# Performance work log

Measured on AMD Instinct MI355X. Metric: run time of the kernel, lower is better.

## Reference

```python
import jax, jax.numpy as jnp
import numpy as np

N_NODES = 110
C = 4096  # in_channels = hidden = out_channels


def setup_inputs() -> dict:
    key = jax.random.key(0)
    ks = jax.random.split(key, 8)
    x = jax.random.normal(ks[0], (N_NODES, C), dtype=jnp.float32)
    adj = jax.random.randint(ks[1], (N_NODES, N_NODES), 0, 2, dtype=jnp.int32)
    # torch.nn.Linear weights stored [out_features, in_features]
    W2 = jax.random.normal(ks[2], (C, C), dtype=jnp.float32) / np.sqrt(C)
    b2 = jax.random.normal(ks[3], (C,), dtype=jnp.float32) * 0.01
    W1 = jax.random.normal(ks[4], (2 * C, C), dtype=jnp.float32) / np.sqrt(2 * C)
    b1 = jax.random.normal(ks[5], (C,), dtype=jnp.float32) * 0.01
    Wl = jax.random.normal(ks[6], (N_NODES, N_NODES), dtype=jnp.float32) / np.sqrt(N_NODES)
    bl = jax.random.normal(ks[7], (N_NODES,), dtype=jnp.float32) * 0.01
    # note: W1 is stored [in=2C, out=C]; W2 [in=C, out=C]; Wl [in=110, out=110]
    return {"x": x, "adj": adj, "W2": W2, "b2": b2, "W1": W1, "b1": b1, "Wl": Wl, "bl": bl}


def reference(x, adj, W2, b2, W1, b1, Wl, bl):
    # FeatGraphConv: h = lin2(x)
    h = x @ W2 + b2  # [N, C]
    # edge_index.nonzero(): adjacency -> edge list (i=src, j=dst); mean-aggregate
    # h[src] at dst. Dense equivalent: column-normalized mask matmul.
    mask = (adj != 0).astype(x.dtype)  # [N, N]
    deg = mask.sum(axis=0)  # in-degree of each target node j
    aggr = (mask.T @ h) / jnp.maximum(deg, 1.0)[:, None]  # [N, C]; 0 for isolated nodes (PyG mean)
    # update: lin1(cat(h, aggr)) then relu (in RegGNN.forward)
    out = jax.nn.relu(jnp.concatenate([h, aggr], axis=1) @ W1 + b1)  # [N, C]
    # x.t(); lin(110,110); x.t()
    out = (out.T @ Wl.T + bl).T  # [N, C]
    return out
```

## Files before the change

kernel.cpp:

```cpp
#include <hip/hip_runtime.h>
#include <hip/hip_fp16.h>

#define C 4096
#define NN 110
#define MPAD 112
#define BN 128
#define BK 64
#define KCHUNK 512
#define LDSTR 72

typedef _Float16 f16x8 __attribute__((ext_vector_type(8)));
typedef float fx4 __attribute__((ext_vector_type(4)));

__global__ void prep1_kernel(const float* __restrict__ x, _Float16* __restrict__ A1) {
    int idx = blockIdx.x * 256 + threadIdx.x;
    int n = idx >> 12;
    float v = (n < NN) ? x[idx] : 0.f;
    A1[idx] = (_Float16)v;
}

__global__ __launch_bounds__(256, 2)
void mm_kernel(const _Float16* __restrict__ A, const float* __restrict__ B,
               float* __restrict__ Cacc, int lda) {
    __shared__ _Float16 As[MPAD * LDSTR];
    __shared__ _Float16 Bs[BN * LDSTR];

    const int t  = threadIdx.x;
    const int j0 = blockIdx.x * BN;
    const int k0 = blockIdx.y * KCHUNK;
    const int w   = t >> 6;
    const int L   = t & 63;
    const int l15 = L & 15;
    const int q   = L >> 4;

    const int bc  = t & 127;
    const int bgq = t >> 7;

    fx4 acc[7][2];
    #pragma unroll
    for (int mt = 0; mt < 7; ++mt)
        #pragma unroll
        for (int nt = 0; nt < 2; ++nt)
            acc[mt][nt] = (fx4){0.f, 0.f, 0.f, 0.f};

    for (int kc = 0; kc < KCHUNK; kc += BK) {
        {
            int idx = t;
            #pragma unroll
            for (int i = 0; i < 4; ++i) {
                if (idx < MPAD * (BK / 8)) {
                    int row = idx >> 3;
                    int ko  = (idx & 7) << 3;
                    *(f16x8*)(As + row * LDSTR + ko) =
                        *(const f16x8*)(A + (size_t)row * lda + k0 + kc + ko);
                }
                idx += 256;
            }
        }
        {
            #pragma unroll
            for (int p = 0; p < 16; ++p) {
                int r = (bgq * 16 + p) * 2;
                float v0 = B[(size_t)(k0 + kc + r) * C + j0 + bc];
                float v1 = B[(size_t)(k0 + kc + r + 1) * C + j0 + bc];
                union { _Float16 h[2]; unsigned u; } pk;
                pk.h[0] = (_Float16)v0;
                pk.h[1] = (_Float16)v1;
                *(unsigned*)(Bs + bc * LDSTR + r) = pk.u;
            }
        }
        __syncthreads();
        #pragma unroll
        for (int s = 0; s < 2; ++s) {
            const int ko = s * 32 + q * 8;
            f16x8 bfrag[2];
            #pragma unroll
            for (int nt = 0; nt < 2; ++nt)
                bfrag[nt] = *(const f16x8*)(Bs + (w * 32 + nt * 16 + l15) * LDSTR + ko);
            #pragma unroll
            for (int mt = 0; mt < 7; ++mt) {
                f16x8 afrag = *(const f16x8*)(As + (mt * 16 + l15) * LDSTR + ko);
                #pragma unroll
                for (int nt = 0; nt < 2; ++nt)
                    acc[mt][nt] = __builtin_amdgcn_mfma_f32_16x16x32_f16(
                        afrag, bfrag[nt], acc[mt][nt], 0, 0, 0);
            }
        }
        __syncthreads();
    }

    #pragma unroll
    for (int mt = 0; mt < 7; ++mt) {
        #pragma unroll
        for (int nt = 0; nt < 2; ++nt) {
            const int col = j0 + w * 32 + nt * 16 + l15;
            #pragma unroll
            for (int r = 0; r < 4; ++r) {
                int row = mt * 16 + q * 4 + r;
                if (row < NN)
                    atomicAdd(&Cacc[(size_t)row * C + col], acc[mt][nt][r]);
            }
        }
    }
}

__global__ __launch_bounds__(256)
void agg_kernel(const float* __restrict__ h_raw, const int* __restrict__ adj,
                const float* __restrict__ b2, _Float16* __restrict__ A3) {
    __shared__ float hb[NN * 16];
    __shared__ unsigned long long mlo[NN], mhi[NN];
    __shared__ float degs[NN];
    const int t  = threadIdx.x;
    const int c0 = blockIdx.x * 16;

    for (int idx = t; idx < NN * 16; idx += 256) {
        int n = idx >> 4, c = idx & 15;
        float v = h_raw[(size_t)n * C + c0 + c] + b2[c0 + c];
        hb[idx] = v;
        A3[(size_t)n * (2 * C) + c0 + c] = (_Float16)v;
    }
    if (t < 64) {
        int n  = NN + (t >> 5);
        int hs = (t >> 4) & 1;
        int c  = t & 15;
        A3[(size_t)n * (2 * C) + hs * C + c0 + c] = (_Float16)0.f;
    }
    if (t < NN) {
        int j = t;
        unsigned long long lo = 0, hi = 0;
        int dg = 0;
        for (int i = 0; i < 64; ++i) {
            int m = (adj[i * NN + j] != 0);
            lo |= ((unsigned long long)m) << i; dg += m;
        }
        for (int i = 64; i < NN; ++i) {
            int m = (adj[i * NN + j] != 0);
            hi |= ((unsigned long long)m) << (i - 64); dg += m;
        }
        mlo[j] = lo; mhi[j] = hi;
        degs[j] = (float)(dg > 0 ? dg : 1);
    }
    __syncthreads();
    for (int idx = t; idx < NN * 16; idx += 256) {
        int j = idx >> 4, c = idx & 15;
        unsigned long long lo = mlo[j], hi = mhi[j];
        float a = 0.f;
        for (int i = 0; i < 64; ++i)
            if ((lo >> i) & 1) a += hb[i * 16 + c];
        for (int i = 64; i < NN; ++i)
            if ((hi >> (i - 64)) & 1) a += hb[i * 16 + c];
        A3[(size_t)j * (2 * C) + C + c0 + c] = (_Float16)(a / degs[j]);
    }
}

__global__ __launch_bounds__(256)
void fin_kernel(const float* __restrict__ z_raw, const float* __restrict__ b1,
                const float* __restrict__ Wl, const float* __restrict__ bl,
                float* __restrict__ out) {
    __shared__ float zs[NN * 64];
    const int t  = threadIdx.x;
    const int c0 = blockIdx.x * 64;
    const int j  = blockIdx.y * 4 + (t >> 6);
    const int c  = t & 63;

    for (int idx = t; idx < NN * 64; idx += 256) {
        int k = idx >> 6, cc = idx & 63;
        float v = z_raw[(size_t)k * C + c0 + cc] + b1[c0 + cc];
        zs[idx] = fmaxf(v, 0.f);
    }
    __syncthreads();
    if (j < NN) {
        float a = bl[j];
        #pragma unroll 2
        for (int k = 0; k < NN; ++k)
            a += Wl[j * NN + k] * zs[k * 64 + c];
        out[(size_t)j * C + c0 + c] = a;
    }
}

extern "C" void kernel_launch(void* const* d_in, const int* in_sizes, int n_in,
                              void* d_out, int out_size, void* d_ws, size_t ws_size,
                              hipStream_t stream) {
    const float* x   = (const float*)d_in[0];
    const int*   adj = (const int*)d_in[1];
    const float* W2  = (const float*)d_in[2];
    const float* b2  = (const float*)d_in[3];
    const float* W1  = (const float*)d_in[4];
    const float* b1  = (const float*)d_in[5];
    const float* Wl  = (const float*)d_in[6];
    const float* bl  = (const float*)d_in[7];
    float* out = (float*)d_out;

    char* ws = (char*)d_ws;
    float*    h_raw = (float*)(ws);
    float*    z_raw = (float*)(ws + 1802240);
    _Float16* A1    = (_Float16*)(ws + 3604480);
    _Float16* A3    = (_Float16*)(ws + 4521984);

    hipMemsetAsync(d_ws, 0, 3604480, stream);
    prep1_kernel<<<(MPAD * C) / 256, 256, 0, stream>>>(x, A1);
    mm_kernel<<<dim3(C / BN, C / KCHUNK), 256, 0, stream>>>(A1, W2, h_raw, C);
    agg_kernel<<<C / 16, 256, 0, stream>>>(h_raw, adj, b2, A3);
    mm_kernel<<<dim3(C / BN, (2 * C) / KCHUNK), 256, 0, stream>>>(A3, W1, z_raw, 2 * C);
    fin_kernel<<<dim3(C / 64, 28), 256, 0, stream>>>(z_raw, b1, Wl, bl, out);
}
```

Before: 381.5 us.

## Double-buffer GEMM LDS with register prefetch and XOR-swizzled B tile

The GEMM kernel now prefetches the next K-slice of A and B into registers while MFMAs run on the current LDS buffer, then commits into a second LDS buffer. This hides global load latency behind compute. The B tile drops its padded stride in favour of an XOR swizzle to avoid LDS bank conflicts. Smaller changes vectorise the prep and aggregation kernels to two elements per thread and cut fin_kernel's grid so each block reuses its staged z tile for 28 output rows instead of 4. The cost is more registers (32 floats plus A vectors) and double the LDS in the GEMM, which may reduce occupancy.

After: 358.7 us. -6.0%, faster.

```diff
diff --git a/kernel.cpp b/kernel.cpp
--- a/kernel.cpp
+++ b/kernel.cpp
@@ -7,101 +7,139 @@
 #define BN 128
 #define BK 64
 #define KCHUNK 512
+#define NIT (KCHUNK / BK)
 #define LDSTR 72
+#define BSTR 64
 
 typedef _Float16 f16x8 __attribute__((ext_vector_type(8)));
 typedef float fx4 __attribute__((ext_vector_type(4)));
 
-__global__ void prep1_kernel(const float* __restrict__ x, _Float16* __restrict__ A1) {
+__global__ __launch_bounds__(256)
+void prep1_kernel(const float* __restrict__ x, _Float16* __restrict__ A1) {
     int idx = blockIdx.x * 256 + threadIdx.x;
-    int n = idx >> 12;
-    float v = (n < NN) ? x[idx] : 0.f;
-    A1[idx] = (_Float16)v;
+    int n = idx >> 11;
+    union { _Float16 h[2]; unsigned u; } pk;
+    pk.u = 0;
+    if (n < NN) {
+        float2 v = *(const float2*)(x + 2 * (size_t)idx);
+        pk.h[0] = (_Float16)v.x;
+        pk.h[1] = (_Float16)v.y;
+    }
+    ((unsigned*)A1)[idx] = pk.u;
 }
 
 __global__ __launch_bounds__(256, 2)
 void mm_kernel(const _Float16* __restrict__ A, const float* __restrict__ B,
                float* __restrict__ Cacc, int lda) {
-    __shared__ _Float16 As[MPAD * LDSTR];
-    __shared__ _Float16 Bs[BN * LDSTR];
-
-    const int t  = threadIdx.x;
-    const int j0 = blockIdx.x * BN;
-    const int k0 = blockIdx.y * KCHUNK;
-    const int w   = t >> 6;
-    const int L   = t & 63;
-    const int l15 = L & 15;
-    const int q   = L >> 4;
-
-    const int bc  = t & 127;
-    const int bgq = t >> 7;
+    __shared__ _Float16 As[2][MPAD * LDSTR];
+    __shared__ _Float16 Bs[2][BN * BSTR];
+
+    const int t    = threadIdx.x;
+    const int j0   = blockIdx.x * BN;
+    const int k0   = blockIdx.y * KCHUNK;
+    const int w    = t >> 6;
+    const int L    = t & 63;
+    const int l15  = L & 15;
+    const int q    = L >> 4;
+    const int bc   = t & 127;
+    const int bgq  = t >> 7;
+    const int bswz = bc & 7;
+
+    int arow[4], ako[4];
+    bool aval[4];
+#pragma unroll
+    for (int i = 0; i < 4; ++i) {
+        int idx = t + i * 256;
+        aval[i] = (idx < MPAD * (BK / 8));
+        int id2 = aval[i] ? idx : 0;
+        arow[i] = id2 >> 3;
+        ako[i]  = (id2 & 7) << 3;
+    }
 
     fx4 acc[7][2];
-    #pragma unroll
+#pragma unroll
     for (int mt = 0; mt < 7; ++mt)
-        #pragma unroll
+#pragma unroll
         for (int nt = 0; nt < 2; ++nt)
             acc[mt][nt] = (fx4){0.f, 0.f, 0.f, 0.f};
 
-    for (int kc = 0; kc < KCHUNK; kc += BK) {
-        {
-            int idx = t;
-            #pragma unroll
-            for (int i = 0; i < 4; ++i) {
-                if (idx < MPAD * (BK / 8)) {
-                    int row = idx >> 3;
-                    int ko  = (idx & 7) << 3;
-                    *(f16x8*)(As + row * LDSTR + ko) =
-                        *(const f16x8*)(A + (size_t)row * lda + k0 + kc + ko);
-                }
-                idx += 256;
-            }
-        }
-        {
-            #pragma unroll
-            for (int p = 0; p < 16; ++p) {
-                int r = (bgq * 16 + p) * 2;
-                float v0 = B[(size_t)(k0 + kc + r) * C + j0 + bc];
-                float v1 = B[(size_t)(k0 + kc + r + 1) * C + j0 + bc];
-                union { _Float16 h[2]; unsigned u; } pk;
-                pk.h[0] = (_Float16)v0;
-                pk.h[1] = (_Float16)v1;
-                *(unsigned*)(Bs + bc * LDSTR + r) = pk.u;
-            }
-        }
-        __syncthreads();
-        #pragma unroll
+    f16x8 av[4];
+    float bv[32];
+
+#define STAGE(kc_)                                                             \
+    {                                                                          \
+        _Pragma("unroll")                                                      \
+        for (int i = 0; i < 4; ++i)                                            \
+            av[i] = *(const f16x8*)(A + (size_t)arow[i] * lda + (k0 + (kc_)) + ako[i]); \
+        _Pragma("unroll")                                                      \
+        for (int p = 0; p < 16; ++p) {                                         \
+            int r = (bgq * 16 + p) * 2;                                        \
+            bv[2 * p]     = B[(size_t)(k0 + (kc_) + r) * C + j0 + bc];         \
+            bv[2 * p + 1] = B[(size_t)(k0 + (kc_) + r + 1) * C + j0 + bc];     \
+        }                                                                      \
+    }
+
+#define COMMIT(b_)                                                             \
+    {                                                                          \
+        _Pragma("unroll")                                                      \
+        for (int i = 0; i < 4; ++i)                                            \
+            if (aval[i])                                                       \
+                *(f16x8*)(As[b_] + arow[i] * LDSTR + ako[i]) = av[i];          \
+        _Pragma("unroll")                                                      \
+        for (int p = 0; p < 16; ++p) {                                         \
+            int P = bgq * 16 + p;                                              \
+            union { _Float16 h[2]; unsigned u; } pk;                           \
+            pk.h[0] = (_Float16)bv[2 * p];                                     \
+            pk.h[1] = (_Float16)bv[2 * p + 1];                                 \
+            *(unsigned*)(Bs[b_] + bc * BSTR + (((P >> 2) ^ bswz) << 3)         \
+                         + ((P & 3) << 1)) = pk.u;                             \
+        }                                                                      \
+    }
+
+    STAGE(0);
+    COMMIT(0);
+    __syncthreads();
+
+    for (int it = 0; it < NIT; ++it) {
+        if (it + 1 < NIT) STAGE((it + 1) * BK);
+        const int b = it & 1;
+#pragma unroll
         for (int s = 0; s < 2; ++s) {
             const int ko = s * 32 + q * 8;
             f16x8 bfrag[2];
-            #pragma unroll
-            for (int nt = 0; nt < 2; ++nt)
-                bfrag[nt] = *(const f16x8*)(Bs + (w * 32 + nt * 16 + l15) * LDSTR + ko);
-            #pragma unroll
+#pragma unroll
+            for (int nt = 0; nt < 2; ++nt) {
+                const int cW = w * 32 + nt * 16 + l15;
+                bfrag[nt] = *(const f16x8*)(Bs[b] + cW * BSTR
+                                + ((((s << 2) + q) ^ (l15 & 7)) << 3));
+            }
+#pragma unroll
             for (int mt = 0; mt < 7; ++mt) {
-                f16x8 afrag = *(const f16x8*)(As + (mt * 16 + l15) * LDSTR + ko);
-                #pragma unroll
+                f16x8 afrag = *(const f16x8*)(As[b] + (mt * 16 + l15) * LDSTR + ko);
+#pragma unroll
                 for (int nt = 0; nt < 2; ++nt)
                     acc[mt][nt] = __builtin_amdgcn_mfma_f32_16x16x32_f16(
                         afrag, bfrag[nt], acc[mt][nt], 0, 0, 0);
             }
         }
+        if (it + 1 < NIT) COMMIT((it + 1) & 1);
         __syncthreads();
     }
 
-    #pragma unroll
-    for (int mt = 0; mt < 7; ++mt) {
-        #pragma unroll
+#pragma unroll
+    for (int mt = 0; mt < 7; ++mt)
+#pragma unroll
         for (int nt = 0; nt < 2; ++nt) {
             const int col = j0 + w * 32 + nt * 16 + l15;
-            #pragma unroll
+#pragma unroll
             for (int r = 0; r < 4; ++r) {
                 int row = mt * 16 + q * 4 + r;
                 if (row < NN)
                     atomicAdd(&Cacc[(size_t)row * C + col], acc[mt][nt][r]);
             }
         }
-    }
+#undef STAGE
+#undef COMMIT
 }
 
 __global__ __launch_bounds__(256)
@@ -113,17 +151,23 @@
     const int t  = threadIdx.x;
     const int c0 = blockIdx.x * 16;
 
-    for (int idx = t; idx < NN * 16; idx += 256) {
-        int n = idx >> 4, c = idx & 15;
-        float v = h_raw[(size_t)n * C + c0 + c] + b2[c0 + c];
-        hb[idx] = v;
-        A3[(size_t)n * (2 * C) + c0 + c] = (_Float16)v;
-    }
-    if (t < 64) {
-        int n  = NN + (t >> 5);
-        int hs = (t >> 4) & 1;
-        int c  = t & 15;
-        A3[(size_t)n * (2 * C) + hs * C + c0 + c] = (_Float16)0.f;
+    for (int idx = t; idx < NN * 8; idx += 256) {
+        int n = idx >> 3, cp = (idx & 7) << 1;
+        float2 v = *(const float2*)(h_raw + (size_t)n * C + c0 + cp);
+        float v0 = v.x + b2[c0 + cp];
+        float v1 = v.y + b2[c0 + cp + 1];
+        hb[n * 16 + cp]     = v0;
+        hb[n * 16 + cp + 1] = v1;
+        union { _Float16 h[2]; unsigned u; } pk;
+        pk.h[0] = (_Float16)v0;
+        pk.h[1] = (_Float16)v1;
+        *(unsigned*)(A3 + (size_t)n * (2 * C) + c0 + cp) = pk.u;
+    }
+    if (t < 32) {
+        int n  = NN + (t >> 4);
+        int hs = (t >> 3) & 1;
+        int cp = (t & 7) << 1;
+        *(unsigned*)(A3 + (size_t)n * (2 * C) + hs * C + c0 + cp) = 0u;
     }
     if (t < NN) {
         int j = t;
@@ -141,15 +185,18 @@
         degs[j] = (float)(dg > 0 ? dg : 1);
     }
     __syncthreads();
-    for (int idx = t; idx < NN * 16; idx += 256) {
-        int j = idx >> 4, c = idx & 15;
+    for (int idx = t; idx < NN * 8; idx += 256) {
+        int j = idx >> 3, cp = (idx & 7) << 1;
         unsigned long long lo = mlo[j], hi = mhi[j];
-        float a = 0.f;
+        float a0 = 0.f, a1 = 0.f;
         for (int i = 0; i < 64; ++i)
-            if ((lo >> i) & 1) a += hb[i * 16 + c];
+            if ((lo >> i) & 1) { a0 += hb[i * 16 + cp]; a1 += hb[i * 16 + cp + 1]; }
         for (int i = 64; i < NN; ++i)
-            if ((hi >> (i - 64)) & 1) a += hb[i * 16 + c];
-        A3[(size_t)j * (2 * C) + C + c0 + c] = (_Float16)(a / degs[j]);
+            if ((hi >> (i - 64)) & 1) { a0 += hb[i * 16 + cp]; a1 += hb[i * 16 + cp + 1]; }
+        union { _Float16 h[2]; unsigned u; } pk;
+        pk.h[0] = (_Float16)(a0 / degs[j]);
+        pk.h[1] = (_Float16)(a1 / degs[j]);
+        *(unsigned*)(A3 + (size_t)j * (2 * C) + C + c0 + cp) = pk.u;
     }
 }
 
@@ -160,7 +207,6 @@
     __shared__ float zs[NN * 64];
     const int t  = threadIdx.x;
     const int c0 = blockIdx.x * 64;
-    const int j  = blockIdx.y * 4 + (t >> 6);
     const int c  = t & 63;
 
     for (int idx = t; idx < NN * 64; idx += 256) {
@@ -169,12 +215,15 @@
         zs[idx] = fmaxf(v, 0.f);
     }
     __syncthreads();
-    if (j < NN) {
-        float a = bl[j];
-        #pragma unroll 2
-        for (int k = 0; k < NN; ++k)
-            a += Wl[j * NN + k] * zs[k * 64 + c];
-        out[(size_t)j * C + c0 + c] = a;
+    for (int jj = 0; jj < 7; ++jj) {
+        int j = blockIdx.y * 28 + jj * 4 + (t >> 6);
+        if (j < NN) {
+            float a = bl[j];
+#pragma unroll 2
+            for (int k = 0; k < NN; ++k)
+                a += Wl[j * NN + k] * zs[k * 64 + c];
+            out[(size_t)j * C + c0 + c] = a;
+        }
     }
 }
 
@@ -198,9 +247,9 @@
     _Float16* A3    = (_Float16*)(ws + 4521984);
 
     hipMemsetAsync(d_ws, 0, 3604480, stream);
-    prep1_kernel<<<(MPAD * C) / 256, 256, 0, stream>>>(x, A1);
+    prep1_kernel<<<(MPAD * C / 2) / 256, 256, 0, stream>>>(x, A1);
     mm_kernel<<<dim3(C / BN, C / KCHUNK), 256, 0, stream>>>(A1, W2, h_raw, C);
     agg_kernel<<<C / 16, 256, 0, stream>>>(h_raw, adj, b2, A3);
     mm_kernel<<<dim3(C / BN, (2 * C) / KCHUNK), 256, 0, stream>>>(A3, W1, z_raw, 2 * C);
-    fin_kernel<<<dim3(C / 64, 28), 256, 0, stream>>>(z_raw, b1, Wl, bl, out);
-}
+    fin_kernel<<<dim3(C / 64, 4), 256, 0, stream>>>(z_raw, b1, Wl, bl, out);
+}
```
